# Performance work log

Hardware: AMD Instinct MI355X
Metric: run time of the kernel (lower is better)

The kernel has to match this reference:

```python
import jax, jax.numpy as jnp
import numpy as np

B, T, EEG, GEO, TH, HID, OUT = 4096, 320, 64, 18, 32, 16, 4
THETA0, BETA, TAU_A, TAU_M, EPS = 0.5, 1.8, 0.36, 0.8, 1e-5


@jax.custom_vjp
def spike_fn(x):
    return jnp.where(x >= 0, 1.0, 0.0).astype(x.dtype)

def _spike_fwd(x):
    return spike_fn(x), x

def _spike_bwd(x, g):
    # SuperSpike-style surrogate gradient (original defvjp not shown in source)
    return (g / (10.0 * jnp.abs(x) + 1.0) ** 2,)

spike_fn.defvjp(_spike_fwd, _spike_bwd)


def setup_inputs() -> dict:
    key = jax.random.key(0)
    ks = jax.random.split(key, 20)
    rn = lambda k, s, sc=0.05: (jax.random.normal(k, s, jnp.float32) * sc)
    return {
        "x_eeg": jax.random.normal(ks[0], (B, T, EEG), jnp.float32),
        "x_geo": jax.random.normal(ks[1], (B, T, GEO), jnp.float32),
        "conv1_k": rn(ks[2], (5, EEG, TH)),   # (W, Cin, Cout)
        "conv1_b": jnp.zeros((TH,), jnp.float32),
        "bn1_scale": jnp.ones((TH,), jnp.float32),
        "bn1_bias": jnp.zeros((TH,), jnp.float32),
        "bn1_mean": rn(ks[3], (TH,)),
        "bn1_var": jnp.abs(rn(ks[4], (TH,))) + 1.0,
        "conv2_k": rn(ks[5], (3, TH, HID)),
        "conv2_b": jnp.zeros((HID,), jnp.float32),
        "bn2_scale": jnp.ones((HID,), jnp.float32),
        "bn2_bias": jnp.zeros((HID,), jnp.float32),
        "bn2_mean": rn(ks[6], (HID,)),
        "bn2_var": jnp.abs(rn(ks[7], (HID,))) + 1.0,
        "geo_W": rn(ks[8], (GEO, HID), 0.2),
        "geo_b": jnp.zeros((HID,), jnp.float32),
        "gamma": jnp.full((HID,), 0.5, jnp.float32),
        "fc1_W": rn(ks[9], (HID * 10, 64), 0.1),
        "fc1_b": jnp.zeros((64,), jnp.float32),
        "fc2_W": rn(ks[10], (64, OUT), 0.1),
        "fc2_b": jnp.zeros((OUT,), jnp.float32),
    }


def _conv1d(x, k, b, pad):
    # x: (B,T,C) NWC; k: (W,Cin,Cout) WIO
    return jax.lax.conv_general_dilated(
        x, k, window_strides=(1,), padding=[(pad, pad)],
        dimension_numbers=("NWC", "WIO", "NWC")) + b


def _bn(x, scale, bias, mean, var):
    return (x - mean) * jax.lax.rsqrt(var + EPS) * scale + bias


def reference(x_eeg, x_geo, conv1_k, conv1_b, bn1_scale, bn1_bias, bn1_mean,
              bn1_var, conv2_k, conv2_b, bn2_scale, bn2_bias, bn2_mean,
              bn2_var, geo_W, geo_b, gamma, fc1_W, fc1_b, fc2_W, fc2_b):
    x = jax.nn.relu(_bn(_conv1d(x_eeg, conv1_k, conv1_b, 2),
                        bn1_scale, bn1_bias, bn1_mean, bn1_var))
    eeg_encoded = jax.nn.relu(_bn(_conv1d(x, conv2_k, conv2_b, 1),
                                  bn2_scale, bn2_bias, bn2_mean, bn2_var))  # (B,T,HID)
    geo_mod = jax.nn.sigmoid(x_geo @ geo_W + geo_b)  # (B,T,HID)

    def scan_fn(carry, inputs):
        mem_alif, eta, mem_li, prev_spike = carry
        cur_eeg, cur_geo = inputs
        eta = TAU_A * eta + (1.0 - TAU_A) * prev_spike
        theta_t = THETA0 + BETA * eta - gamma * cur_geo
        mem_alif = TAU_M * mem_alif + cur_eeg
        spk = spike_fn(mem_alif - theta_t)
        mem_alif = mem_alif * (1.0 - spk)
        mem_li = 0.9 * mem_li + spk
        return (mem_alif, eta, mem_li, spk), mem_li

    z = jnp.zeros((B, HID), jnp.float32)
    _, mem_li_seq = jax.lax.scan(
        scan_fn, (z, z, z, z),
        (jnp.swapaxes(eeg_encoded, 0, 1), jnp.swapaxes(geo_mod, 0, 1)))
    mem_li_seq = jnp.swapaxes(jnp.swapaxes(mem_li_seq, 0, 1), 1, 2)  # (B,HID,T)

    windows = mem_li_seq.reshape(B, HID, 10, 32)
    dp_feat = (jnp.mean(windows[..., 16:], axis=-1) -
               jnp.mean(windows[..., :16], axis=-1)).reshape(B, -1)  # (B,160)
    out = jax.nn.relu(dp_feat @ fc1_W + fc1_b)
    return out @ fc2_W + fc2_b
```

## Files before the change

### kernel.cpp

```cpp
#include <hip/hip_runtime.h>

typedef _Float16 f16;
typedef __attribute__((ext_vector_type(8))) _Float16 f16x8;
typedef __attribute__((ext_vector_type(16))) float f32x16;

#define T_LEN 320

__device__ __forceinline__ void split2h(float v, unsigned short &h, unsigned short &l) {
    f16 hh = (f16)v;
    f16 ll = (f16)((v - (float)hh) * 4096.0f);
    h = __builtin_bit_cast(unsigned short, hh);
    l = __builtin_bit_cast(unsigned short, ll);
}

__global__ __launch_bounds__(256) void geo_prep_kernel(
    const float* __restrict__ k1, const float* __restrict__ c1b,
    const float* __restrict__ bn1s, const float* __restrict__ bn1b,
    const float* __restrict__ bn1m, const float* __restrict__ bn1v,
    const float* __restrict__ k2, const float* __restrict__ c2b,
    const float* __restrict__ bn2s, const float* __restrict__ bn2b,
    const float* __restrict__ bn2m, const float* __restrict__ bn2v,
    unsigned short* __restrict__ w1f, unsigned short* __restrict__ w2f,
    float* __restrict__ sb)
{
    const int tid = threadIdx.x;
    for (int e = tid; e < 20 * 64; e += 256) {
        const int ks = e >> 6, l = e & 63;
        const int lh = l >> 5, n = l & 31;
        for (int j = 0; j < 8; ++j) {
            const int kg = ks * 16 + lh * 8 + j;
            unsigned short h, lo; split2h(k1[kg * 32 + n], h, lo);
            w1f[((ks * 2 + 0) * 64 + l) * 8 + j] = h;
            w1f[((ks * 2 + 1) * 64 + l) * 8 + j] = lo;
        }
    }
    for (int e = tid; e < 6 * 64; e += 256) {
        const int ks = e >> 6, l = e & 63;
        const int lh = l >> 5, n = l & 31;
        for (int j = 0; j < 8; ++j) {
            const int kg = ks * 16 + lh * 8 + j;
            const float v = (n < 16) ? k2[kg * 16 + n] : 0.0f;
            unsigned short h, lo; split2h(v, h, lo);
            w2f[((ks * 2 + 0) * 64 + l) * 8 + j] = h;
            w2f[((ks * 2 + 1) * 64 + l) * 8 + j] = lo;
        }
    }
    if (tid < 32) {
        const float s1 = bn1s[tid] * (1.0f / sqrtf(bn1v[tid] + 1e-5f));
        sb[tid]      = s1;
        sb[32 + tid] = bn1b[tid] + (c1b[tid] - bn1m[tid]) * s1;
    }
    if (tid < 16) {
        const float s2 = bn2s[tid] * (1.0f / sqrtf(bn2v[tid] + 1e-5f));
        sb[64 + tid] = s2;
        sb[80 + tid] = bn2b[tid] + (c2b[tid] - bn2m[tid]) * s2;
    }
}

struct ConvSmem {
    unsigned short xh[70][64], xl[70][64];
    unsigned short c1h[66][40], c1l[66][40];
};

#define MFMA32(A, B, C) __builtin_amdgcn_mfma_f32_32x32x16_f16((A), (B), (C), 0, 0, 0)

__global__ __launch_bounds__(256, 5) void geo_alif_conv_kernel(
    const float* __restrict__ x_eeg,
    const unsigned short* __restrict__ w1f, const unsigned short* __restrict__ w2f,
    const float* __restrict__ sb, float* __restrict__ e_ws)
{
    __shared__ ConvSmem sm;
    const int tid = threadIdx.x, lane = tid & 63, wv = tid >> 6;
    const int l31 = lane & 31, lh = lane >> 5;
    const int row = blockIdx.x / 5, cc = blockIdx.x % 5;
    const int t0 = cc * 64;
    const float* xrow = x_eeg + (size_t)row * (T_LEN * 64);
    float* erow = e_ws + (size_t)row * (16 * T_LEN);

    {
        float4 v[5];
#pragma unroll
        for (int q = 0; q < 5; ++q) {
            const int fi = tid + q * 256;
            float4 tv = {0.f, 0.f, 0.f, 0.f};
            if (fi < 1120) {
                const int s = fi >> 4;
                const int tabs = t0 - 3 + s;
                if (tabs >= 0 && tabs < T_LEN)
                    tv = *reinterpret_cast<const float4*>(xrow + (size_t)tabs * 64 + (fi & 15) * 4);
            }
            v[q] = tv;
        }
#pragma unroll
        for (int q = 0; q < 5; ++q) {
            const int fi = tid + q * 256;
            if (fi < 1120) {
                const int s = fi >> 4, cq = fi & 15;
                unsigned short h0,l0,h1,l1,h2,l2,h3,l3;
                split2h(v[q].x, h0, l0); split2h(v[q].y, h1, l1);
                split2h(v[q].z, h2, l2); split2h(v[q].w, h3, l3);
                const int off = (((cq >> 1) ^ (s & 7)) * 8) + (cq & 1) * 4;
                ushort4 hv = {h0, h1, h2, h3}, lv = {l0, l1, l2, l3};
                *reinterpret_cast<ushort4*>(&sm.xh[s][off]) = hv;
                *reinterpret_cast<ushort4*>(&sm.xl[s][off]) = lv;
            }
        }
    }
    __syncthreads();

    if (wv < 3) {
        const int frag = wv;
        const float s1 = sb[l31], b1 = sb[32 + l31];
        const f16x8* w1v = reinterpret_cast<const f16x8*>(w1f);
        f32x16 am, cx;
#pragma unroll
        for (int q = 0; q < 16; ++q) { am[q] = 0.f; cx[q] = 0.f; }
        f16x8 pbh[4], pbl[4], pah[3], pal[3];
#pragma unroll
        for (int p = 0; p < 4; ++p) {
            pbh[p] = w1v[(p * 2 + 0) * 64 + lane];
            pbl[p] = w1v[(p * 2 + 1) * 64 + lane];
        }
#pragma unroll
        for (int p = 0; p < 3; ++p) {
            const int kb = p * 16 + lh * 8;
            int s = frag * 32 + l31 + (kb >> 6); if (s > 69) s = 69;
            const int off = ((((kb & 63) >> 3) ^ (s & 7)) * 8);
            pah[p] = *reinterpret_cast<const f16x8*>(&sm.xh[s][off]);
            pal[p] = *reinterpret_cast<const f16x8*>(&sm.xl[s][off]);
        }
#pragma unroll
        for (int ks = 0; ks < 20; ++ks) {
            const f16x8 ah = pah[ks % 3], al = pal[ks % 3];
            const f16x8 bh = pbh[ks % 4], bl = pbl[ks % 4];
            am = MFMA32(ah, bh, am);
            cx = MFMA32(ah, bl, cx);
            cx = MFMA32(al, bh, cx);
            if (ks < 17) {
                const int kb = (ks + 3) * 16 + lh * 8;
                int s = frag * 32 + l31 + (kb >> 6); if (s > 69) s = 69;
                const int off = ((((kb & 63) >> 3) ^ (s & 7)) * 8);
                pah[ks % 3] = *reinterpret_cast<const f16x8*>(&sm.xh[s][off]);
                pal[ks % 3] = *reinterpret_cast<const f16x8*>(&sm.xl[s][off]);
            }
            if (ks < 16) {
                pbh[ks % 4] = w1v[((ks + 4) * 2 + 0) * 64 + lane];
                pbl[ks % 4] = w1v[((ks + 4) * 2 + 1) * 64 + lane];
            }
        }
#pragma unroll
        for (int reg = 0; reg < 16; ++reg) {
            const int rl = frag * 32 + (reg & 3) + 8 * (reg >> 2) + 4 * lh;
            if (rl < 66) {
                const int tabs = t0 - 1 + rl;
                float v = am[reg] + cx[reg] * (1.0f / 4096.0f);
                v = (tabs >= 0 && tabs < T_LEN) ? fmaxf(v * s1 + b1, 0.0f) : 0.0f;
                unsigned short h_, lo_; split2h(v, h_, lo_);
                const int ui = (((l31 >> 3) ^ (rl & 3)) * 8) + (l31 & 7);
                sm.c1h[rl][ui] = h_;
                sm.c1l[rl][ui] = lo_;
            }
        }
    }
    __syncthreads();

    if (wv < 2) {
        const int mf = wv;
        const float s2 = (l31 < 16) ? sb[64 + l31] : 0.0f;
        const float b2 = (l31 < 16) ? sb[80 + l31] : 0.0f;
        const f16x8* w2v = reinterpret_cast<const f16x8*>(w2f);
        f16x8 w2hv[6], w2lv[6];
#pragma unroll
        for (int p = 0; p < 6; ++p) {
            w2hv[p] = w2v[(p * 2 + 0) * 64 + lane];
            w2lv[p] = w2v[(p * 2 + 1) * 64 + lane];
        }
        f32x16 am, cx;
#pragma unroll
        for (int q = 0; q < 16; ++q) { am[q] = 0.f; cx[q] = 0.f; }
#pragma unroll
        for (int ks = 0; ks < 6; ++ks) {
            const int kb = ks * 16 + lh * 8;
            const int sidx = mf * 32 + l31 + (kb >> 5);
            const int off = ((((kb & 31) >> 3) ^ (sidx & 3)) * 8);
            f16x8 ah = *reinterpret_cast<const f16x8*>(&sm.c1h[sidx][off]);
            f16x8 al = *reinterpret_cast<const f16x8*>(&sm.c1l[sidx][off]);
            am = MFMA32(ah, w2hv[ks], am);
            cx = MFMA32(ah, w2lv[ks], cx);
            cx = MFMA32(al, w2hv[ks], cx);
        }
        if (l31 < 16) {
#pragma unroll
            for (int g = 0; g < 4; ++g) {
                const int t = t0 + mf * 32 + 8 * g + 4 * lh;
                float4 ov;
                ov.x = fmaxf((am[g*4+0] + cx[g*4+0] * (1.0f/4096.0f)) * s2 + b2, 0.0f);
                ov.y = fmaxf((am[g*4+1] + cx[g*4+1] * (1.0f/4096.0f)) * s2 + b2, 0.0f);
                ov.z = fmaxf((am[g*4+2] + cx[g*4+2] * (1.0f/4096.0f)) * s2 + b2, 0.0f);
                ov.w = fmaxf((am[g*4+3] + cx[g*4+3] * (1.0f/4096.0f)) * s2 + b2, 0.0f);
                *reinterpret_cast<float4*>(erow + (size_t)l31 * T_LEN + t) = ov;
            }
        }
    }
}

__global__ __launch_bounds__(256) void geo_alif_scan_kernel(
    const float* __restrict__ e_ws, const float* __restrict__ x_geo,
    const float* __restrict__ geoW, const float* __restrict__ geob,
    const float* __restrict__ gam,
    const float* __restrict__ fc1W, const float* __restrict__ fc1b,
    const float* __restrict__ fc2W, const float* __restrict__ fc2b,
    float* __restrict__ out)
{
    __shared__ float gW[18][16];
    __shared__ float geo_s[16][16][16];
    __shared__ float dp[16][160];
    __shared__ float h1s[16][64];

    const int tid = threadIdx.x;
    for (int i = tid; i < 288; i += 256) gW[i / 16][i & 15] = geoW[i];
    __syncthreads();

    const int r = tid >> 4, h = tid & 15;
    const int b = blockIdx.x * 16 + r;
    const float* ep = e_ws + ((size_t)b * 16 + h) * T_LEN;
    const float gmv = gam[h];

    float mem = 0.f, eta = 0.f, li = 0.f, prev = 0.f, acc = 0.f;

    for (int c = 0; c < 20; ++c) {
        const float* ec = ep + c * 16;
        float4 ev0 = *reinterpret_cast<const float4*>(ec);
        float4 ev1 = *reinterpret_cast<const float4*>(ec + 4);
        float4 ev2 = *reinterpret_cast<const float4*>(ec + 8);
        float4 ev3 = *reinterpret_cast<const float4*>(ec + 12);

        {
            const int rg = tid >> 4, tl = tid & 15;
            const int t = c * 16 + tl;
            const float* xg = x_geo + ((size_t)(blockIdx.x * 16 + rg) * T_LEN + t) * 18;
            float xv[18];
#pragma unroll
            for (int i = 0; i < 18; ++i) xv[i] = xg[i];
#pragma unroll
            for (int hh = 0; hh < 16; ++hh) {
                float a = geob[hh];
#pragma unroll
                for (int i = 0; i < 18; ++i) a = fmaf(xv[i], gW[i][hh], a);
                geo_s[rg][tl][hh] = 1.f / (1.f + expf(-a));
            }
        }
        __syncthreads();

        float evs[16] = {ev0.x, ev0.y, ev0.z, ev0.w, ev1.x, ev1.y, ev1.z, ev1.w,
                         ev2.x, ev2.y, ev2.z, ev2.w, ev3.x, ev3.y, ev3.z, ev3.w};
#pragma unroll
        for (int u = 0; u < 16; ++u) {
            const int tt = c * 16 + u;
            const float g = geo_s[r][u][h];
            eta = 0.36f * eta + 0.64f * prev;
            const float th = 0.5f + 1.8f * eta - gmv * g;
            mem = 0.8f * mem + evs[u];
            const bool sp = (mem >= th);
            const float spk = sp ? 1.f : 0.f;
            prev = spk;
            mem = sp ? 0.f : mem;
            li = 0.9f * li + spk;
            acc += ((tt & 31) < 16) ? -li : li;
            if ((tt & 31) == 31) {
                dp[r][h * 10 + (tt >> 5)] = acc * 0.0625f;
                acc = 0.f;
            }
        }
        __syncthreads();
    }

    {
        const int rr = tid >> 4, j0 = tid & 15;
        float a0 = fc1b[j0], a1 = fc1b[j0 + 16], a2 = fc1b[j0 + 32], a3 = fc1b[j0 + 48];
        for (int f = 0; f < 160; ++f) {
            const float d = dp[rr][f];
            a0 = fmaf(d, fc1W[f * 64 + j0],      a0);
            a1 = fmaf(d, fc1W[f * 64 + j0 + 16], a1);
            a2 = fmaf(d, fc1W[f * 64 + j0 + 32], a2);
            a3 = fmaf(d, fc1W[f * 64 + j0 + 48], a3);
        }
        h1s[rr][j0]      = fmaxf(a0, 0.f);
        h1s[rr][j0 + 16] = fmaxf(a1, 0.f);
        h1s[rr][j0 + 32] = fmaxf(a2, 0.f);
        h1s[rr][j0 + 48] = fmaxf(a3, 0.f);
    }
    __syncthreads();

    if (tid < 64) {
        const int rr = tid >> 2, o = tid & 3;
        float a = fc2b[o];
#pragma unroll
        for (int j = 0; j < 64; ++j) a = fmaf(h1s[rr][j], fc2W[j * 4 + o], a);
        out[((size_t)(blockIdx.x * 16 + rr)) * 4 + o] = a;
    }
}

extern "C" void kernel_launch(void* const* d_in, const int* in_sizes, int n_in,
                              void* d_out, int out_size, void* d_ws, size_t ws_size,
                              hipStream_t stream) {
    (void)in_sizes; (void)n_in; (void)out_size; (void)ws_size;
    const float* x_eeg = (const float*)d_in[0];
    const float* x_geo = (const float*)d_in[1];
    const float* k1    = (const float*)d_in[2];
    const float* c1b   = (const float*)d_in[3];
    const float* bn1s  = (const float*)d_in[4];
    const float* bn1b  = (const float*)d_in[5];
    const float* bn1m  = (const float*)d_in[6];
    const float* bn1v  = (const float*)d_in[7];
    const float* k2    = (const float*)d_in[8];
    const float* c2b   = (const float*)d_in[9];
    const float* bn2s  = (const float*)d_in[10];
    const float* bn2b  = (const float*)d_in[11];
    const float* bn2m  = (const float*)d_in[12];
    const float* bn2v  = (const float*)d_in[13];
    const float* geoW  = (const float*)d_in[14];
    const float* geob  = (const float*)d_in[15];
    const float* gam   = (const float*)d_in[16];
    const float* fc1W  = (const float*)d_in[17];
    const float* fc1b  = (const float*)d_in[18];
    const float* fc2W  = (const float*)d_in[19];
    const float* fc2b  = (const float*)d_in[20];

    char* wsb = (char*)d_ws;
    unsigned short* w1f = (unsigned short*)(wsb);
    unsigned short* w2f = (unsigned short*)(wsb + 40960);
    float* sb           = (float*)(wsb + 53248);
    float* e_ws         = (float*)(wsb + 65536);

    geo_prep_kernel<<<1, 256, 0, stream>>>(
        k1, c1b, bn1s, bn1b, bn1m, bn1v,
        k2, c2b, bn2s, bn2b, bn2m, bn2v, w1f, w2f, sb);

    geo_alif_conv_kernel<<<4096 * 5, 256, 0, stream>>>(x_eeg, w1f, w2f, sb, e_ws);

    geo_alif_scan_kernel<<<256, 256, 0, stream>>>(
        e_ws, x_geo, geoW, geob, gam, fc1W, fc1b, fc2W, fc2b, (float*)d_out);
}
```

Before: 281.0 us.

## Fuse conv, gate and ALIF scan into one per-row pipelined kernel

Merges the conv kernel and the scan kernel into a single kernel with one block per batch row. The block walks the sequence in 64-step chunks, double-buffering the eeg input tile in shared memory. Wave 3 runs the geo gate and the sequential ALIF scan for the previous chunk while waves 0-2 do the conv MFMAs for the current one, and the FC head runs per row at the end. This removes the global round trip of the encoded activations and one launch. In exchange only 16 lanes of one wave run the serial scan per row, shared memory per block grows, and there are only 4096 blocks with 2 per CU.

```diff
diff --git a/kernel.cpp b/kernel.cpp
--- a/kernel.cpp
+++ b/kernel.cpp
@@ -57,247 +57,275 @@
     }
 }
 
-struct ConvSmem {
-    unsigned short xh[70][64], xl[70][64];
+struct FusedSmem {
+    unsigned short xh[2][70][64], xl[2][70][64];
     unsigned short c1h[66][40], c1l[66][40];
+    float e[2][16][68];
+    float gateT[16][68];
+    float gW[18][16];
+    float dp[160];
+    float h1[64];
 };
 
 #define MFMA32(A, B, C) __builtin_amdgcn_mfma_f32_32x32x16_f16((A), (B), (C), 0, 0, 0)
 
-__global__ __launch_bounds__(256, 5) void geo_alif_conv_kernel(
-    const float* __restrict__ x_eeg,
+__device__ __forceinline__ void gate_scan_chunk(
+    FusedSmem& sm, const float* __restrict__ x_geo,
+    const float* __restrict__ geob, int row, int pc, int lane, float gmv,
+    float& mem, float& eta, float& li, float& prevs, float& acc)
+{
+    const int tg = pc * 64 + lane;
+    const float* xg = x_geo + ((size_t)row * T_LEN + tg) * 18;
+    float xv[18];
+#pragma unroll
+    for (int i = 0; i < 18; ++i) xv[i] = xg[i];
+#pragma unroll
+    for (int hh = 0; hh < 16; ++hh) {
+        float a = geob[hh];
+#pragma unroll
+        for (int i = 0; i < 18; ++i) a = fmaf(xv[i], sm.gW[i][hh], a);
+        sm.gateT[hh][lane] = 1.f / (1.f + expf(-a));
+    }
+    if (lane < 16) {
+        const int h = lane;
+        const int eb = pc & 1;
+#pragma unroll
+        for (int tb = 0; tb < 16; ++tb) {
+            float4 ev = *reinterpret_cast<const float4*>(&sm.e[eb][h][tb * 4]);
+            float4 gv = *reinterpret_cast<const float4*>(&sm.gateT[h][tb * 4]);
+            float evs[4] = {ev.x, ev.y, ev.z, ev.w};
+            float gvs[4] = {gv.x, gv.y, gv.z, gv.w};
+#pragma unroll
+            for (int u = 0; u < 4; ++u) {
+                const int tt = pc * 64 + tb * 4 + u;
+                eta = 0.36f * eta + 0.64f * prevs;
+                const float th = 0.5f + 1.8f * eta - gmv * gvs[u];
+                mem = 0.8f * mem + evs[u];
+                const bool sp = (mem >= th);
+                const float spk = sp ? 1.f : 0.f;
+                prevs = spk;
+                mem = sp ? 0.f : mem;
+                li = 0.9f * li + spk;
+                acc += ((tt & 31) < 16) ? -li : li;
+                if ((tt & 31) == 31) {
+                    sm.dp[h * 10 + (tt >> 5)] = acc * 0.0625f;
+                    acc = 0.f;
+                }
+            }
+        }
+    }
+}
+
+__global__ __launch_bounds__(256, 2) void geo_fused_kernel(
+    const float* __restrict__ x_eeg, const float* __restrict__ x_geo,
     const unsigned short* __restrict__ w1f, const unsigned short* __restrict__ w2f,
-    const float* __restrict__ sb, float* __restrict__ e_ws)
-{
-    __shared__ ConvSmem sm;
-    const int tid = threadIdx.x, lane = tid & 63, wv = tid >> 6;
-    const int l31 = lane & 31, lh = lane >> 5;
-    const int row = blockIdx.x / 5, cc = blockIdx.x % 5;
-    const int t0 = cc * 64;
-    const float* xrow = x_eeg + (size_t)row * (T_LEN * 64);
-    float* erow = e_ws + (size_t)row * (16 * T_LEN);
-
-    {
-        float4 v[5];
-#pragma unroll
-        for (int q = 0; q < 5; ++q) {
-            const int fi = tid + q * 256;
-            float4 tv = {0.f, 0.f, 0.f, 0.f};
-            if (fi < 1120) {
-                const int s = fi >> 4;
-                const int tabs = t0 - 3 + s;
-                if (tabs >= 0 && tabs < T_LEN)
-                    tv = *reinterpret_cast<const float4*>(xrow + (size_t)tabs * 64 + (fi & 15) * 4);
-            }
-            v[q] = tv;
-        }
-#pragma unroll
-        for (int q = 0; q < 5; ++q) {
-            const int fi = tid + q * 256;
-            if (fi < 1120) {
-                const int s = fi >> 4, cq = fi & 15;
-                unsigned short h0,l0,h1,l1,h2,l2,h3,l3;
-                split2h(v[q].x, h0, l0); split2h(v[q].y, h1, l1);
-                split2h(v[q].z, h2, l2); split2h(v[q].w, h3, l3);
-                const int off = (((cq >> 1) ^ (s & 7)) * 8) + (cq & 1) * 4;
-                ushort4 hv = {h0, h1, h2, h3}, lv = {l0, l1, l2, l3};
-                *reinterpret_cast<ushort4*>(&sm.xh[s][off]) = hv;
-                *reinterpret_cast<ushort4*>(&sm.xl[s][off]) = lv;
-            }
-        }
-    }
-    __syncthreads();
-
-    if (wv < 3) {
-        const int frag = wv;
-        const float s1 = sb[l31], b1 = sb[32 + l31];
-        const f16x8* w1v = reinterpret_cast<const f16x8*>(w1f);
-        f32x16 am, cx;
-#pragma unroll
-        for (int q = 0; q < 16; ++q) { am[q] = 0.f; cx[q] = 0.f; }
-        f16x8 pbh[4], pbl[4], pah[3], pal[3];
-#pragma unroll
-        for (int p = 0; p < 4; ++p) {
-            pbh[p] = w1v[(p * 2 + 0) * 64 + lane];
-            pbl[p] = w1v[(p * 2 + 1) * 64 + lane];
-        }
-#pragma unroll
-        for (int p = 0; p < 3; ++p) {
-            const int kb = p * 16 + lh * 8;
-            int s = frag * 32 + l31 + (kb >> 6); if (s > 69) s = 69;
-            const int off = ((((kb & 63) >> 3) ^ (s & 7)) * 8);
-            pah[p] = *reinterpret_cast<const f16x8*>(&sm.xh[s][off]);
-            pal[p] = *reinterpret_cast<const f16x8*>(&sm.xl[s][off]);
-        }
-#pragma unroll
-        for (int ks = 0; ks < 20; ++ks) {
-            const f16x8 ah = pah[ks % 3], al = pal[ks % 3];
-            const f16x8 bh = pbh[ks % 4], bl = pbl[ks % 4];
-            am = MFMA32(ah, bh, am);
-            cx = MFMA32(ah, bl, cx);
-            cx = MFMA32(al, bh, cx);
-            if (ks < 17) {
-                const int kb = (ks + 3) * 16 + lh * 8;
-                int s = frag * 32 + l31 + (kb >> 6); if (s > 69) s = 69;
-                const int off = ((((kb & 63) >> 3) ^ (s & 7)) * 8);
-                pah[ks % 3] = *reinterpret_cast<const f16x8*>(&sm.xh[s][off]);
-                pal[ks % 3] = *reinterpret_cast<const f16x8*>(&sm.xl[s][off]);
-            }
-            if (ks < 16) {
-                pbh[ks % 4] = w1v[((ks + 4) * 2 + 0) * 64 + lane];
-                pbl[ks % 4] = w1v[((ks + 4) * 2 + 1) * 64 + lane];
-            }
-        }
-#pragma unroll
-        for (int reg = 0; reg < 16; ++reg) {
-            const int rl = frag * 32 + (reg & 3) + 8 * (reg >> 2) + 4 * lh;
-            if (rl < 66) {
-                const int tabs = t0 - 1 + rl;
-                float v = am[reg] + cx[reg] * (1.0f / 4096.0f);
-                v = (tabs >= 0 && tabs < T_LEN) ? fmaxf(v * s1 + b1, 0.0f) : 0.0f;
-                unsigned short h_, lo_; split2h(v, h_, lo_);
-                const int ui = (((l31 >> 3) ^ (rl & 3)) * 8) + (l31 & 7);
-                sm.c1h[rl][ui] = h_;
-                sm.c1l[rl][ui] = lo_;
-            }
-        }
-    }
-    __syncthreads();
-
-    if (wv < 2) {
-        const int mf = wv;
-        const float s2 = (l31 < 16) ? sb[64 + l31] : 0.0f;
-        const float b2 = (l31 < 16) ? sb[80 + l31] : 0.0f;
-        const f16x8* w2v = reinterpret_cast<const f16x8*>(w2f);
-        f16x8 w2hv[6], w2lv[6];
-#pragma unroll
-        for (int p = 0; p < 6; ++p) {
-            w2hv[p] = w2v[(p * 2 + 0) * 64 + lane];
-            w2lv[p] = w2v[(p * 2 + 1) * 64 + lane];
-        }
-        f32x16 am, cx;
-#pragma unroll
-        for (int q = 0; q < 16; ++q) { am[q] = 0.f; cx[q] = 0.f; }
-#pragma unroll
-        for (int ks = 0; ks < 6; ++ks) {
-            const int kb = ks * 16 + lh * 8;
-            const int sidx = mf * 32 + l31 + (kb >> 5);
-            const int off = ((((kb & 31) >> 3) ^ (sidx & 3)) * 8);
-            f16x8 ah = *reinterpret_cast<const f16x8*>(&sm.c1h[sidx][off]);
-            f16x8 al = *reinterpret_cast<const f16x8*>(&sm.c1l[sidx][off]);
-            am = MFMA32(ah, w2hv[ks], am);
-            cx = MFMA32(ah, w2lv[ks], cx);
-            cx = MFMA32(al, w2hv[ks], cx);
-        }
-        if (l31 < 16) {
-#pragma unroll
-            for (int g = 0; g < 4; ++g) {
-                const int t = t0 + mf * 32 + 8 * g + 4 * lh;
-                float4 ov;
-                ov.x = fmaxf((am[g*4+0] + cx[g*4+0] * (1.0f/4096.0f)) * s2 + b2, 0.0f);
-                ov.y = fmaxf((am[g*4+1] + cx[g*4+1] * (1.0f/4096.0f)) * s2 + b2, 0.0f);
-                ov.z = fmaxf((am[g*4+2] + cx[g*4+2] * (1.0f/4096.0f)) * s2 + b2, 0.0f);
-                ov.w = fmaxf((am[g*4+3] + cx[g*4+3] * (1.0f/4096.0f)) * s2 + b2, 0.0f);
-                *reinterpret_cast<float4*>(erow + (size_t)l31 * T_LEN + t) = ov;
-            }
-        }
-    }
-}
-
-__global__ __launch_bounds__(256) void geo_alif_scan_kernel(
-    const float* __restrict__ e_ws, const float* __restrict__ x_geo,
+    const float* __restrict__ sb,
     const float* __restrict__ geoW, const float* __restrict__ geob,
     const float* __restrict__ gam,
     const float* __restrict__ fc1W, const float* __restrict__ fc1b,
     const float* __restrict__ fc2W, const float* __restrict__ fc2b,
     float* __restrict__ out)
 {
-    __shared__ float gW[18][16];
-    __shared__ float geo_s[16][16][16];
-    __shared__ float dp[16][160];
-    __shared__ float h1s[16][64];
-
-    const int tid = threadIdx.x;
-    for (int i = tid; i < 288; i += 256) gW[i / 16][i & 15] = geoW[i];
+    __shared__ FusedSmem sm;
+    const int tid = threadIdx.x, lane = tid & 63, wv = tid >> 6;
+    const int l31 = lane & 31, lh = lane >> 5;
+    const int row = blockIdx.x;
+    const float* xrow = x_eeg + (size_t)row * (T_LEN * 64);
+
+    for (int i = tid; i < 288; i += 256) sm.gW[i / 16][i & 15] = geoW[i];
+
+    const float s1 = sb[l31], b1 = sb[32 + l31];
+    const float s2 = (l31 < 16) ? sb[64 + l31] : 0.0f;
+    const float b2 = (l31 < 16) ? sb[80 + l31] : 0.0f;
+    const f16x8* w1v = reinterpret_cast<const f16x8*>(w1f);
+    const f16x8* w2v = reinterpret_cast<const f16x8*>(w2f);
+    f16x8 w2hv[6], w2lv[6];
+    if (wv < 2) {
+#pragma unroll
+        for (int p = 0; p < 6; ++p) {
+            w2hv[p] = w2v[(p * 2 + 0) * 64 + lane];
+            w2lv[p] = w2v[(p * 2 + 1) * 64 + lane];
+        }
+    }
+    float mem = 0.f, eta = 0.f, li = 0.f, prevs = 0.f, acc = 0.f;
+    const float gmv = gam[lane & 15];
+
+    {
+        float4 sv[5];
+#pragma unroll
+        for (int q = 0; q < 5; ++q) {
+            const int fi = tid + q * 256;
+            float4 tv = {0.f, 0.f, 0.f, 0.f};
+            if (fi < 1120) {
+                const int s = fi >> 4;
+                const int tabs = -3 + s;
+                if (tabs >= 0)
+                    tv = *reinterpret_cast<const float4*>(xrow + (size_t)tabs * 64 + (fi & 15) * 4);
+            }
+            sv[q] = tv;
+        }
+#pragma unroll
+        for (int q = 0; q < 5; ++q) {
+            const int fi = tid + q * 256;
+            if (fi < 1120) {
+                const int s = fi >> 4, cq = fi & 15;
+                unsigned short h0,l0,h1,l1,h2,l2,h3,l3;
+                split2h(sv[q].x, h0, l0); split2h(sv[q].y, h1, l1);
+                split2h(sv[q].z, h2, l2); split2h(sv[q].w, h3, l3);
+                const int off = (((cq >> 1) ^ (s & 7)) * 8) + (cq & 1) * 4;
+                ushort4 hv = {h0, h1, h2, h3}, lv = {l0, l1, l2, l3};
+                *reinterpret_cast<ushort4*>(&sm.xh[0][s][off]) = hv;
+                *reinterpret_cast<ushort4*>(&sm.xl[0][s][off]) = lv;
+            }
+        }
+    }
     __syncthreads();
 
-    const int r = tid >> 4, h = tid & 15;
-    const int b = blockIdx.x * 16 + r;
-    const float* ep = e_ws + ((size_t)b * 16 + h) * T_LEN;
-    const float gmv = gam[h];
-
-    float mem = 0.f, eta = 0.f, li = 0.f, prev = 0.f, acc = 0.f;
-
-    for (int c = 0; c < 20; ++c) {
-        const float* ec = ep + c * 16;
-        float4 ev0 = *reinterpret_cast<const float4*>(ec);
-        float4 ev1 = *reinterpret_cast<const float4*>(ec + 4);
-        float4 ev2 = *reinterpret_cast<const float4*>(ec + 8);
-        float4 ev3 = *reinterpret_cast<const float4*>(ec + 12);
-
-        {
-            const int rg = tid >> 4, tl = tid & 15;
-            const int t = c * 16 + tl;
-            const float* xg = x_geo + ((size_t)(blockIdx.x * 16 + rg) * T_LEN + t) * 18;
-            float xv[18];
-#pragma unroll
-            for (int i = 0; i < 18; ++i) xv[i] = xg[i];
-#pragma unroll
-            for (int hh = 0; hh < 16; ++hh) {
-                float a = geob[hh];
-#pragma unroll
-                for (int i = 0; i < 18; ++i) a = fmaf(xv[i], gW[i][hh], a);
-                geo_s[rg][tl][hh] = 1.f / (1.f + expf(-a));
-            }
+    for (int cc = 0; cc < 5; ++cc) {
+        const int buf = cc & 1;
+        const int t0 = cc * 64;
+
+        float4 sv[5];
+        const bool dost = (cc < 4);
+        if (dost) {
+            const int tn = t0 + 64;
+#pragma unroll
+            for (int q = 0; q < 5; ++q) {
+                const int fi = tid + q * 256;
+                float4 tv = {0.f, 0.f, 0.f, 0.f};
+                if (fi < 1120) {
+                    const int s = fi >> 4;
+                    const int tabs = tn - 3 + s;
+                    if (tabs >= 0 && tabs < T_LEN)
+                        tv = *reinterpret_cast<const float4*>(xrow + (size_t)tabs * 64 + (fi & 15) * 4);
+                }
+                sv[q] = tv;
+            }
+        }
+
+        if (wv < 3) {
+            const int frag = wv;
+            f32x16 am, cx;
+#pragma unroll
+            for (int q = 0; q < 16; ++q) { am[q] = 0.f; cx[q] = 0.f; }
+            f16x8 pbh[4], pbl[4], pah[3], pal[3];
+#pragma unroll
+            for (int p = 0; p < 4; ++p) {
+                pbh[p] = w1v[(p * 2 + 0) * 64 + lane];
+                pbl[p] = w1v[(p * 2 + 1) * 64 + lane];
+            }
+#pragma unroll
+            for (int p = 0; p < 3; ++p) {
+                const int kb = p * 16 + lh * 8;
+                int s = frag * 32 + l31 + (kb >> 6); if (s > 69) s = 69;
+                const int off = ((((kb & 63) >> 3) ^ (s & 7)) * 8);
+                pah[p] = *reinterpret_cast<const f16x8*>(&sm.xh[buf][s][off]);
+                pal[p] = *reinterpret_cast<const f16x8*>(&sm.xl[buf][s][off]);
+            }
+#pragma unroll
+            for (int ks = 0; ks < 20; ++ks) {
+                const f16x8 ah = pah[ks % 3], al = pal[ks % 3];
+                const f16x8 bh = pbh[ks % 4], bl = pbl[ks % 4];
+                am = MFMA32(ah, bh, am);
+                cx = MFMA32(ah, bl, cx);
+                cx = MFMA32(al, bh, cx);
+                if (ks < 17) {
+                    const int kb = (ks + 3) * 16 + lh * 8;
+                    int s = frag * 32 + l31 + (kb >> 6); if (s > 69) s = 69;
+                    const int off = ((((kb & 63) >> 3) ^ (s & 7)) * 8);
+                    pah[ks % 3] = *reinterpret_cast<const f16x8*>(&sm.xh[buf][s][off]);
+                    pal[ks % 3] = *reinterpret_cast<const f16x8*>(&sm.xl[buf][s][off]);
+                }
+                if (ks < 16) {
+                    pbh[ks % 4] = w1v[((ks + 4) * 2 + 0) * 64 + lane];
+                    pbl[ks % 4] = w1v[((ks + 4) * 2 + 1) * 64 + lane];
+                }
+            }
+#pragma unroll
+            for (int reg = 0; reg < 16; ++reg) {
+                const int rl = frag * 32 + (reg & 3) + 8 * (reg >> 2) + 4 * lh;
+                if (rl < 66) {
+                    const int tabs = t0 - 1 + rl;
+                    float v = am[reg] + cx[reg] * (1.0f / 4096.0f);
+                    v = (tabs >= 0 && tabs < T_LEN) ? fmaxf(v * s1 + b1, 0.0f) : 0.0f;
+                    unsigned short h_, lo_; split2h(v, h_, lo_);
+                    const int ui = (((l31 >> 3) ^ (rl & 3)) * 8) + (l31 & 7);
+                    sm.c1h[rl][ui] = h_;
+                    sm.c1l[rl][ui] = lo_;
+                }
+            }
+        } else if (cc >= 1) {
+            gate_scan_chunk(sm, x_geo, geob, row, cc - 1, lane, gmv,
+                            mem, eta, li, prevs, acc);
         }
         __syncthreads();
 
-        float evs[16] = {ev0.x, ev0.y, ev0.z, ev0.w, ev1.x, ev1.y, ev1.z, ev1.w,
-                         ev2.x, ev2.y, ev2.z, ev2.w, ev3.x, ev3.y, ev3.z, ev3.w};
-#pragma unroll
-        for (int u = 0; u < 16; ++u) {
-            const int tt = c * 16 + u;
-            const float g = geo_s[r][u][h];
-            eta = 0.36f * eta + 0.64f * prev;
-            const float th = 0.5f + 1.8f * eta - gmv * g;
-            mem = 0.8f * mem + evs[u];
-            const bool sp = (mem >= th);
-            const float spk = sp ? 1.f : 0.f;
-            prev = spk;
-            mem = sp ? 0.f : mem;
-            li = 0.9f * li + spk;
-            acc += ((tt & 31) < 16) ? -li : li;
-            if ((tt & 31) == 31) {
-                dp[r][h * 10 + (tt >> 5)] = acc * 0.0625f;
-                acc = 0.f;
+        if (wv < 2) {
+            const int mf = wv;
+            f32x16 am, cx;
+#pragma unroll
+            for (int q = 0; q < 16; ++q) { am[q] = 0.f; cx[q] = 0.f; }
+#pragma unroll
+            for (int ks = 0; ks < 6; ++ks) {
+                const int kb = ks * 16 + lh * 8;
+                const int sidx = mf * 32 + l31 + (kb >> 5);
+                const int off = ((((kb & 31) >> 3) ^ (sidx & 3)) * 8);
+                f16x8 ah = *reinterpret_cast<const f16x8*>(&sm.c1h[sidx][off]);
+                f16x8 al = *reinterpret_cast<const f16x8*>(&sm.c1l[sidx][off]);
+                am = MFMA32(ah, w2hv[ks], am);
+                cx = MFMA32(ah, w2lv[ks], cx);
+                cx = MFMA32(al, w2hv[ks], cx);
+            }
+            if (l31 < 16) {
+#pragma unroll
+                for (int g = 0; g < 4; ++g) {
+                    const int tloc = mf * 32 + 8 * g + 4 * lh;
+                    float4 ov;
+                    ov.x = fmaxf((am[g*4+0] + cx[g*4+0] * (1.0f/4096.0f)) * s2 + b2, 0.0f);
+                    ov.y = fmaxf((am[g*4+1] + cx[g*4+1] * (1.0f/4096.0f)) * s2 + b2, 0.0f);
+                    ov.z = fmaxf((am[g*4+2] + cx[g*4+2] * (1.0f/4096.0f)) * s2 + b2, 0.0f);
+                    ov.w = fmaxf((am[g*4+3] + cx[g*4+3] * (1.0f/4096.0f)) * s2 + b2, 0.0f);
+                    *reinterpret_cast<float4*>(&sm.e[buf][l31][tloc]) = ov;
+                }
+            }
+        }
+        if (dost) {
+#pragma unroll
+            for (int q = 0; q < 5; ++q) {
+                const int fi = tid + q * 256;
+                if (fi < 1120) {
+                    const int s = fi >> 4, cq = fi & 15;
+                    unsigned short h0,l0,h1,l1,h2,l2,h3,l3;
+                    split2h(sv[q].x, h0, l0); split2h(sv[q].y, h1, l1);
+                    split2h(sv[q].z, h2, l2); split2h(sv[q].w, h3, l3);
+                    const int off = (((cq >> 1) ^ (s & 7)) * 8) + (cq & 1) * 4;
+                    ushort4 hv = {h0, h1, h2, h3}, lv = {l0, l1, l2, l3};
+                    *reinterpret_cast<ushort4*>(&sm.xh[buf ^ 1][s][off]) = hv;
+                    *reinterpret_cast<ushort4*>(&sm.xl[buf ^ 1][s][off]) = lv;
+                }
             }
         }
         __syncthreads();
     }
 
-    {
-        const int rr = tid >> 4, j0 = tid & 15;
-        float a0 = fc1b[j0], a1 = fc1b[j0 + 16], a2 = fc1b[j0 + 32], a3 = fc1b[j0 + 48];
-        for (int f = 0; f < 160; ++f) {
-            const float d = dp[rr][f];
-            a0 = fmaf(d, fc1W[f * 64 + j0],      a0);
-            a1 = fmaf(d, fc1W[f * 64 + j0 + 16], a1);
-            a2 = fmaf(d, fc1W[f * 64 + j0 + 32], a2);
-            a3 = fmaf(d, fc1W[f * 64 + j0 + 48], a3);
-        }
-        h1s[rr][j0]      = fmaxf(a0, 0.f);
-        h1s[rr][j0 + 16] = fmaxf(a1, 0.f);
-        h1s[rr][j0 + 32] = fmaxf(a2, 0.f);
-        h1s[rr][j0 + 48] = fmaxf(a3, 0.f);
-    }
+    if (wv == 3)
+        gate_scan_chunk(sm, x_geo, geob, row, 4, lane, gmv,
+                        mem, eta, li, prevs, acc);
     __syncthreads();
 
-    if (tid < 64) {
-        const int rr = tid >> 2, o = tid & 3;
-        float a = fc2b[o];
-#pragma unroll
-        for (int j = 0; j < 64; ++j) a = fmaf(h1s[rr][j], fc2W[j * 4 + o], a);
-        out[((size_t)(blockIdx.x * 16 + rr)) * 4 + o] = a;
+    if (wv == 0) {
+        const int j = lane;
+        float a = fc1b[j];
+        for (int f = 0; f < 160; ++f) a = fmaf(sm.dp[f], fc1W[f * 64 + j], a);
+        sm.h1[j] = fmaxf(a, 0.f);
+    }
+    __syncthreads();
+
+    if (tid < 4) {
+        float a = fc2b[tid];
+#pragma unroll
+        for (int j = 0; j < 64; ++j) a = fmaf(sm.h1[j], fc2W[j * 4 + tid], a);
+        out[(size_t)row * 4 + tid] = a;
     }
 }
 
@@ -331,14 +359,12 @@
     unsigned short* w1f = (unsigned short*)(wsb);
     unsigned short* w2f = (unsigned short*)(wsb + 40960);
     float* sb           = (float*)(wsb + 53248);
-    float* e_ws         = (float*)(wsb + 65536);
 
     geo_prep_kernel<<<1, 256, 0, stream>>>(
         k1, c1b, bn1s, bn1b, bn1m, bn1v,
         k2, c2b, bn2s, bn2b, bn2m, bn2v, w1f, w2f, sb);
 
-    geo_alif_conv_kernel<<<4096 * 5, 256, 0, stream>>>(x_eeg, w1f, w2f, sb, e_ws);
-
-    geo_alif_scan_kernel<<<256, 256, 0, stream>>>(
-        e_ws, x_geo, geoW, geob, gam, fc1W, fc1b, fc2W, fc2b, (float*)d_out);
-}
+    geo_fused_kernel<<<4096, 256, 0, stream>>>(
+        x_eeg, x_geo, w1f, w2f, sb, geoW, geob, gam,
+        fc1W, fc1b, fc2W, fc2b, (float*)d_out);
+}
```

Measured after the change: 738.7 us. +162.9%, slower.
